# Kernel optimization log

Hardware: AMD Instinct MI355X
Metric: run time of the kernel (lower is better)

The kernel has to match this reference:

```python
import jax, jax.numpy as jnp
import numpy as np

B, S, H, V, C = 32, 512, 256, 50000, 5
NUM_LAYERS, WINDOW = 2, 2


def setup_inputs() -> dict:
    key = jax.random.key(0)
    ks = jax.random.split(key, 24)
    std = 0.1  # matches nn.init.normal_(p, 0, 0.1)
    n = lambda k, shp: jax.random.normal(k, shp, dtype=jnp.float32) * std
    u = lambda k, shp: -0.05 + jax.random.uniform(k, shp, dtype=jnp.float32) * 0.1
    return {
        "input_sentences": jax.random.randint(ks[0], (B, S), 0, V),
        "sentences_length": jax.random.randint(ks[1], (B,), 1, S),
        "hh0": u(ks[2], (B, S, H)),
        "cs0": u(ks[3], (B, S, H)),
        "embed": n(ks[4], (V, H)),
        # stacked word-gate weights, gate order: i, l, r, f, s, output, u
        "W_lr": n(ks[5], (7, H, 2 * H)),
        "W_c": n(ks[6], (7, H, H)),
        "W_x": n(ks[7], (7, H, H)),
        "W_g": n(ks[8], (7, H, H)),
        "gate_bias": n(ks[9], (7, H)),
        # sentence-state gates
        "W_fg_g": n(ks[10], (H, H)),
        "W_fg_h": n(ks[11], (H, H)),
        "W_fgi_g": n(ks[12], (H, H)),
        "W_fgi_h": n(ks[13], (H, H)),
        "W_og_g": n(ks[14], (H, H)),
        "W_og_h": n(ks[15], (H, H)),
        "b_fg": n(ks[16], (H,)),
        "b_fgi": n(ks[17], (H,)),
        # output head
        "W1": n(ks[18], (H, 2 * H)),
        "b1": n(ks[19], (H,)),
        "Wout": n(ks[20], (C, H)),
        "bout": n(ks[21], (C,)),
    }


def _before_sum(x, window):
    # sum of right-shifted (zero-padded at front) copies, shifts 1..window
    out = jnp.zeros_like(x)
    for s in range(1, window + 1):
        out = out + jnp.pad(x[:, :-s], ((0, 0), (s, 0), (0, 0)))
    return out


def _after_sum(x, window):
    out = jnp.zeros_like(x)
    for s in range(1, window + 1):
        out = out + jnp.pad(x[:, s:], ((0, 0), (0, s), (0, 0)))
    return out


def _slstm_step(hh, cs, sv, scs, wv, W_lr, W_c, W_x, W_g, gate_bias,
                W_fg_g, W_fg_h, W_fgi_g, W_fgi_h, W_og_g, W_og_h, b_fg, b_fgi):
    avg_hh = hh.mean(axis=1)                                   # [B,H]
    f_hat_g = jax.nn.sigmoid(sv @ W_fg_g.T + avg_hh @ W_fg_h.T + b_fg)
    # NOTE: original code (faithfully) uses output_gate_bias here, not output_gate_g_bias
    og_g = jax.nn.sigmoid(sv @ W_og_g.T + avg_hh @ W_og_h.T + gate_bias[5])
    f_hat_g_i = jax.nn.sigmoid((sv @ W_fgi_g.T)[:, None] + hh @ W_fgi_h.T + b_fgi)
    scores = jax.nn.softmax(f_hat_g_i, axis=2)                 # over hidden dim
    new_scs = jax.nn.softmax(f_hat_g, axis=1) * scs + (scores * cs).sum(axis=1)
    new_sv = og_g * jnp.tanh(new_scs)

    hb = _before_sum(hh, WINDOW)
    ha = _after_sum(hh, WINDOW)
    cb = _before_sum(cs, WINDOW)
    ca = _after_sum(cs, WINDOW)
    ba = jnp.concatenate([hb, ha], axis=-1)                    # [B,S,2H]

    # all 7 gate pre-activations at once: [B,S,7,H]
    pre = (jnp.einsum('bsk,ghk->bsgh', ba, W_lr)
           + jnp.einsum('bsk,ghk->bsgh', hh, W_c)
           + jnp.einsum('bsk,ghk->bsgh', wv, W_x)
           + (jnp.einsum('bk,ghk->bgh', new_sv, W_g) + gate_bias)[:, None])

    g5 = jax.nn.sigmoid(pre[..., :5, :])                       # i,l,r,f,s
    b_, s_ = g5.shape[:2]
    # joint softmax over the concatenated 5*H gate vector (as in torch cat+softmax)
    g5 = jax.nn.softmax(g5.reshape(b_, s_, -1), axis=-1).reshape(b_, s_, 5, -1)
    i_t, l_t, r_t, f_t, s_t = (g5[..., k, :] for k in range(5))
    og = jax.nn.sigmoid(pre[..., 5, :])
    u_g = jnp.tanh(pre[..., 6, :])

    new_cs = l_t * cb + f_t * cs + r_t * ca + s_t * scs[:, None] + i_t * u_g
    new_hh = og * jnp.tanh(new_cs)
    return new_hh, new_cs, new_sv, new_scs


def reference(input_sentences, sentences_length, hh0, cs0, embed,
              W_lr, W_c, W_x, W_g, gate_bias,
              W_fg_g, W_fg_h, W_fgi_g, W_fgi_h, W_og_g, W_og_h, b_fg, b_fgi,
              W1, b1, Wout, bout):
    wv = embed[input_sentences]                                # [B,S,H]
    hh, cs = hh0, cs0
    sv, scs = hh0.mean(axis=1), cs0.mean(axis=1)
    for _ in range(NUM_LAYERS):
        hh, cs, sv, scs = _slstm_step(hh, cs, sv, scs, wv,
                                      W_lr, W_c, W_x, W_g, gate_bias,
                                      W_fg_g, W_fg_h, W_fgi_g, W_fgi_h,
                                      W_og_g, W_og_h, b_fg, b_fgi)
    avg_hh = hh.mean(axis=1)
    conc = jnp.concatenate([avg_hh, sv], axis=1) @ W1.T + b1
    fc = conc @ Wout.T + bout
    return jax.nn.log_softmax(fc, axis=1), sv
```

## Files before the change

### kernel.cpp

```cpp
#include <hip/hip_runtime.h>
#include <stdint.h>
#include <math.h>

#define B_   32
#define S_   512
#define H_   256
#define M_   (B_*S_)
#define KBIG 1024
#define NB   1792
#define C_   5

typedef __bf16 bf16;
typedef __bf16 bf16x8 __attribute__((ext_vector_type(8)));
typedef float  floatx4 __attribute__((ext_vector_type(4)));

__device__ __forceinline__ float sigm(float x){ return 1.f/(1.f+expf(-x)); }

__device__ __forceinline__ void gl16(const bf16* g, bf16* l){
    __builtin_amdgcn_global_load_lds(
        (const __attribute__((address_space(1))) unsigned int*)g,
        (__attribute__((address_space(3))) unsigned int*)l, 16, 0, 0);
}

__global__ void wcomb_k(const float* __restrict__ Wlr, const float* __restrict__ Wc,
                        const float* __restrict__ Wx, bf16* __restrict__ WT){
    int n = blockIdx.x;
    int g = n >> 8, h = n & 255;
    int k4 = threadIdx.x * 4;
    const float* src;
    if (k4 < 512)      src = Wlr + ((size_t)(g*256 + h))*512 + k4;
    else if (k4 < 768) src = Wc  + ((size_t)(g*256 + h))*256 + (k4 - 512);
    else               src = Wx  + ((size_t)(g*256 + h))*256 + (k4 - 768);
    float4 v = *(const float4*)src;
    bf16 o[4] = {(bf16)v.x,(bf16)v.y,(bf16)v.z,(bf16)v.w};
    *(uint2*)&WT[(size_t)n*KBIG + k4] = *(uint2*)o;
}

__global__ void cvtw_k(const float* __restrict__ a, bf16* __restrict__ o){
    int i4 = (blockIdx.x*256 + threadIdx.x)*4;
    float4 v = *(const float4*)(a + i4);
    bf16 t[4] = {(bf16)v.x,(bf16)v.y,(bf16)v.z,(bf16)v.w};
    *(uint2*)(o + i4) = *(uint2*)t;
}

__global__ void gather_k(const int* __restrict__ idx, const float* __restrict__ embed,
                         bf16* __restrict__ wv){
    int i4 = (blockIdx.x*256 + threadIdx.x)*4;
    int m = i4 >> 8, h = i4 & 255;
    float4 v = *(const float4*)(embed + (size_t)idx[m]*H_ + h);
    bf16 o[4] = {(bf16)v.x,(bf16)v.y,(bf16)v.z,(bf16)v.w};
    *(uint2*)(wv + (size_t)m*H_ + h) = *(uint2*)o;
}

__global__ void mean1_k(const float* __restrict__ x, float* __restrict__ part){
    int b = blockIdx.x, c = blockIdx.y, h = threadIdx.x;
    const float* p = x + ((size_t)b*S_ + c*32)*H_ + h;
    float s = 0.f;
    #pragma unroll 8
    for (int t=0;t<32;t++) s += p[(size_t)t*H_];
    part[((size_t)b*16 + c)*H_ + h] = s;
}
__global__ void mean2_k(const float* __restrict__ part, float* __restrict__ out){
    int b = blockIdx.x, h = threadIdx.x;
    float s = 0.f;
    #pragma unroll
    for (int c=0;c<16;c++) s += part[((size_t)b*16 + c)*H_ + h];
    out[b*H_ + h] = s * (1.f/512.f);
}

__global__ void buildx_k(const float* __restrict__ hh, const bf16* __restrict__ wv,
                         bf16* __restrict__ X){
    int m = blockIdx.x, h = threadIdx.x;
    int s = m & (S_-1);
    size_t base = (size_t)m*H_ + h;
    float hb = (s>=1    ? hh[base - H_] : 0.f) + (s>=2    ? hh[base - 2*H_] : 0.f);
    float ha = (s<=S_-2 ? hh[base + H_] : 0.f) + (s<=S_-3 ? hh[base + 2*H_] : 0.f);
    bf16* xr = X + (size_t)m*KBIG;
    xr[h]     = (bf16)hb;
    xr[256+h] = (bf16)ha;
    xr[512+h] = (bf16)hh[base];
    xr[768+h] = wv[base];
}

__global__ void mv5_k(const float* __restrict__ sv, const float* __restrict__ avg,
    const float* __restrict__ Wfg_g, const float* __restrict__ Wfg_h,
    const float* __restrict__ Wog_g, const float* __restrict__ Wog_h,
    const float* __restrict__ Wfgi_g, float* __restrict__ res){
    int j = blockIdx.x, b = blockIdx.y, h = threadIdx.x;
    const float* vec = (j==1 || j==3) ? avg + b*H_ : sv + b*H_;
    const float* W   = (j==0)?Wfg_g:(j==1)?Wfg_h:(j==2)?Wog_g:(j==3)?Wog_h:Wfgi_g;
    __shared__ float v[H_];
    v[h] = vec[h]; __syncthreads();
    const float* w = W + (size_t)h*H_;
    float d = 0.f;
    for (int k=0;k<H_;k++) d += v[k]*w[k];
    res[((size_t)b*5 + j)*H_ + h] = d;
}
__global__ void comb_k(const float* __restrict__ res, const float* __restrict__ b_fg,
                       const float* __restrict__ gbias, const float* __restrict__ b_fgi,
                       float* __restrict__ fhg, float* __restrict__ ogg,
                       float* __restrict__ svg){
    int b = blockIdx.x, h = threadIdx.x;
    const float* r = res + (size_t)b*5*H_;
    fhg[b*H_+h] = sigm(r[h] + r[H_+h] + b_fg[h]);
    ogg[b*H_+h] = sigm(r[2*H_+h] + r[3*H_+h] + gbias[5*H_+h]);
    svg[b*H_+h] = r[4*H_+h] + b_fgi[h];
}

template<int EPI>
__global__ __launch_bounds__(256)
void mgemm_k(const bf16* __restrict__ A, const bf16* __restrict__ BT,
             bf16* __restrict__ C, const float* __restrict__ gt,
             int Kdim, int lda, int ldb, int ldc){
    __shared__ alignas(16) bf16 lsA[128*32];
    __shared__ alignas(16) bf16 lsB[128*32];
    int tid  = threadIdx.x;
    int m0 = blockIdx.y * 128, n0 = blockIdx.x * 128;
    int wave = tid >> 6, lane = tid & 63;
    int wm = (wave & 1) * 64, wn = (wave >> 1) * 64;
    int lrow = lane & 15, quad = lane >> 4;

    floatx4 zero = {0.f,0.f,0.f,0.f};
    floatx4 acc[4][4];
    #pragma unroll
    for (int i=0;i<4;i++)
        #pragma unroll
        for (int j=0;j<4;j++) acc[i][j] = zero;

    int srow = tid >> 2;
    int scol = (tid & 3) * 8;
    const bf16* Abase = A  + (size_t)(m0 + srow)*lda + scol;
    const bf16* Bbase = BT + (size_t)(n0 + srow)*ldb + scol;
    bf16* dA0 = &lsA[srow*32 + scol];
    bf16* dA1 = &lsA[(64+srow)*32 + scol];
    bf16* dB0 = &lsB[srow*32 + scol];
    bf16* dB1 = &lsB[(64+srow)*32 + scol];

    for (int k0 = 0; k0 < Kdim; k0 += 32){
        __syncthreads();
        gl16(Abase + k0,                     dA0);
        gl16(Abase + (size_t)64*lda + k0,    dA1);
        gl16(Bbase + k0,                     dB0);
        gl16(Bbase + (size_t)64*ldb + k0,    dB1);
        __syncthreads();
        bf16x8 af[4], bfr[4];
        #pragma unroll
        for (int mi=0;mi<4;mi++) af[mi]  = *(const bf16x8*)&lsA[(wm+mi*16+lrow)*32 + quad*8];
        #pragma unroll
        for (int ni=0;ni<4;ni++) bfr[ni] = *(const bf16x8*)&lsB[(wn+ni*16+lrow)*32 + quad*8];
        #pragma unroll
        for (int mi=0;mi<4;mi++)
            #pragma unroll
            for (int ni=0;ni<4;ni++)
                acc[mi][ni] = __builtin_amdgcn_mfma_f32_16x16x32_bf16(af[mi], bfr[ni], acc[mi][ni], 0, 0, 0);
    }

    #pragma unroll
    for (int mi=0;mi<4;mi++)
        #pragma unroll
        for (int ni=0;ni<4;ni++){
            int row = m0 + wm + mi*16 + quad*4;
            int col = n0 + wn + ni*16 + lrow;
            #pragma unroll
            for (int r=0;r<4;r++){
                float v = acc[mi][ni][r];
                if (EPI) v += gt[(size_t)((row+r)>>9)*NB + col];
                C[(size_t)(row+r)*ldc + col] = (bf16)v;
            }
        }
}

__global__ void scorep_k(const bf16* __restrict__ fgih, const float* __restrict__ svg,
                         const float* __restrict__ cs, float* __restrict__ part){
    int chunk = blockIdx.x, b = blockIdx.y;
    int tid = threadIdx.x, wave = tid >> 6, lane = tid & 63;
    __shared__ float acc4[4][256];
    float sw[4], acc[4] = {0.f,0.f,0.f,0.f};
    #pragma unroll
    for (int j=0;j<4;j++) sw[j] = svg[b*H_ + lane + 64*j];
    for (int t=wave; t<16; t+=4){
        int m = b*S_ + chunk*16 + t;
        const bf16* fr = fgih + (size_t)m*H_;
        float e[4], loc = 0.f;
        #pragma unroll
        for (int j=0;j<4;j++){ e[j] = expf(sigm(sw[j] + (float)fr[lane+64*j])); loc += e[j]; }
        #pragma unroll
        for (int off=32; off; off>>=1) loc += __shfl_xor(loc, off, 64);
        float inv = 1.f/loc;
        const float* cr = cs + (size_t)m*H_;
        #pragma unroll
        for (int j=0;j<4;j++) acc[j] += e[j]*inv*cr[lane+64*j];
    }
    #pragma unroll
    for (int j=0;j<4;j++) acc4[wave][lane+64*j] = acc[j];
    __syncthreads();
    part[((size_t)b*32 + chunk)*H_ + tid] =
        acc4[0][tid] + acc4[1][tid] + acc4[2][tid] + acc4[3][tid];
}

__global__ void newscs_k(const float* __restrict__ part, const float* __restrict__ fhg,
                         const float* __restrict__ ogg, const float* __restrict__ scs_in,
                         float* __restrict__ scs_out, float* __restrict__ sv_out){
    int b = blockIdx.x, h = threadIdx.x;
    __shared__ float r[256];
    float dot = 0.f;
    #pragma unroll 8
    for (int c=0;c<32;c++) dot += part[((size_t)b*32+c)*H_ + h];
    float e = expf(fhg[b*H_+h]);
    r[h] = e; __syncthreads();
    for (int off=128; off; off>>=1){ if (h<off) r[h] += r[h+off]; __syncthreads(); }
    float ns = (e / r[0]) * scs_in[b*H_+h] + dot;
    scs_out[b*H_+h] = ns;
    sv_out[b*H_+h]  = ogg[b*H_+h] * tanhf(ns);
}

__global__ void gterm_k(const float* __restrict__ svn, const float* __restrict__ Wg,
                        const float* __restrict__ gbias, float* __restrict__ gt){
    int g = blockIdx.x, b = blockIdx.y, h = threadIdx.x;
    __shared__ float s[H_];
    s[h] = svn[b*H_+h]; __syncthreads();
    const float* w = Wg + ((size_t)g*H_ + h)*H_;
    float d = 0.f;
    for (int k=0;k<H_;k++) d += s[k]*w[k];
    gt[(size_t)b*NB + g*H_ + h] = d + gbias[g*H_+h];
}

__global__ void gates_k(const bf16* __restrict__ pre, const float* __restrict__ cs_in,
                        const float* __restrict__ scs_in,
                        float* __restrict__ hh_out, float* __restrict__ cs_out){
    int tid = threadIdx.x, wave = tid >> 6, lane = tid & 63;
    int m = blockIdx.x*4 + wave;
    int b = m >> 9, s = m & (S_-1);
    const bf16* row = pre + (size_t)m*NB;
    float ex[4][5], og[4], u[4];
    float loc = 0.f;
    #pragma unroll
    for (int j=0;j<4;j++){
        int h = lane + 64*j;
        #pragma unroll
        for (int g=0; g<5; ++g){
            float e = expf(sigm((float)row[g*H_ + h]));
            ex[j][g] = e; loc += e;
        }
        og[j] = sigm((float)row[5*H_ + h]);
        u[j]  = tanhf((float)row[6*H_ + h]);
    }
    #pragma unroll
    for (int off=32; off; off>>=1) loc += __shfl_xor(loc, off, 64);
    float inv = 1.f / loc;
    #pragma unroll
    for (int j=0;j<4;j++){
        int h = lane + 64*j;
        size_t i = (size_t)m*H_ + h;
        float cb = (s>=1    ? cs_in[i - H_] : 0.f) + (s>=2    ? cs_in[i - 2*H_] : 0.f);
        float ca = (s<=S_-2 ? cs_in[i + H_] : 0.f) + (s<=S_-3 ? cs_in[i + 2*H_] : 0.f);
        float nc = ex[j][1]*inv*cb + ex[j][3]*inv*cs_in[i] + ex[j][2]*inv*ca
                 + ex[j][4]*inv*scs_in[b*H_+h] + ex[j][0]*inv*u[j];
        cs_out[i] = nc;
        hh_out[i] = og[j] * tanhf(nc);
    }
}

__global__ void head_k(const float* __restrict__ avgh, const float* __restrict__ sv,
                       const float* __restrict__ W1, const float* __restrict__ b1,
                       const float* __restrict__ Wout, const float* __restrict__ bout,
                       float* __restrict__ out){
    int b = blockIdx.x, t = threadIdx.x;
    __shared__ float conc[H_];
    __shared__ float fc[8];
    const float* wr = W1 + (size_t)t*512;
    float d = b1[t];
    for (int k=0;k<H_;k++) d += avgh[b*H_+k]*wr[k];
    for (int k=0;k<H_;k++) d += sv[b*H_+k]*wr[256+k];
    conc[t] = d;
    __syncthreads();
    if (t < C_){
        const float* wo = Wout + (size_t)t*H_;
        float s = bout[t];
        for (int i=0;i<H_;i++) s += conc[i]*wo[i];
        fc[t] = s;
    }
    __syncthreads();
    if (t == 0){
        float mx = fc[0];
        for (int c=1;c<C_;c++) mx = fmaxf(mx, fc[c]);
        float se = 0.f;
        for (int c=0;c<C_;c++) se += expf(fc[c]-mx);
        float lse = mx + logf(se);
        for (int c=0;c<C_;c++) out[b*C_+c] = fc[c]-lse;
    }
    out[B_*C_ + b*H_ + t] = sv[b*H_+t];
}

extern "C" void kernel_launch(void* const* d_in, const int* in_sizes, int n_in,
                              void* d_out, int out_size, void* d_ws, size_t ws_size,
                              hipStream_t stream){
    const int*   idx    = (const int*)d_in[0];
    const float* hh0    = (const float*)d_in[2];
    const float* cs0    = (const float*)d_in[3];
    const float* embed  = (const float*)d_in[4];
    const float* Wlr    = (const float*)d_in[5];
    const float* Wc     = (const float*)d_in[6];
    const float* Wx     = (const float*)d_in[7];
    const float* Wg     = (const float*)d_in[8];
    const float* gbias  = (const float*)d_in[9];
    const float* Wfg_g  = (const float*)d_in[10];
    const float* Wfg_h  = (const float*)d_in[11];
    const float* Wfgi_g = (const float*)d_in[12];
    const float* Wfgi_h = (const float*)d_in[13];
    const float* Wog_g  = (const float*)d_in[14];
    const float* Wog_h  = (const float*)d_in[15];
    const float* b_fg   = (const float*)d_in[16];
    const float* b_fgi  = (const float*)d_in[17];
    const float* W1     = (const float*)d_in[18];
    const float* b1     = (const float*)d_in[19];
    const float* Wout   = (const float*)d_in[20];
    const float* bout   = (const float*)d_in[21];

    uint8_t* p = (uint8_t*)d_ws;
    auto alloc = [&](size_t bytes)->void*{ void* r=(void*)p; p += (bytes + 255) & ~(size_t)255; return r; };
    bf16*  WT    = (bf16*)alloc((size_t)NB*KBIG*2);
    bf16*  WfgiT = (bf16*)alloc((size_t)H_*H_*2);
    bf16*  X     = (bf16*)alloc((size_t)M_*KBIG*2);
    bf16*  wv    = (bf16*)alloc((size_t)M_*H_*2);
    bf16*  pre   = (bf16*)alloc((size_t)M_*NB*2);
    bf16*  fgih  = (bf16*)alloc((size_t)M_*H_*2);
    float* hhA = (float*)alloc((size_t)M_*H_*4);
    float* csA = (float*)alloc((size_t)M_*H_*4);
    float* hhB = (float*)alloc((size_t)M_*H_*4);
    float* csB = (float*)alloc((size_t)M_*H_*4);
    float* mpart= (float*)alloc((size_t)B_*16*H_*4);
    float* part = (float*)alloc((size_t)B_*32*H_*4);
    float* res5 = (float*)alloc((size_t)B_*5*H_*4);
    float* avgh = (float*)alloc(B_*H_*4);
    float* fhg  = (float*)alloc(B_*H_*4);
    float* ogg  = (float*)alloc(B_*H_*4);
    float* svg  = (float*)alloc(B_*H_*4);
    float* svP0 = (float*)alloc(B_*H_*4);
    float* svP1 = (float*)alloc(B_*H_*4);
    float* scP0 = (float*)alloc(B_*H_*4);
    float* scP1 = (float*)alloc(B_*H_*4);
    float* gt   = (float*)alloc((size_t)B_*NB*4);

    wcomb_k <<<NB,          256, 0, stream>>>(Wlr, Wc, Wx, WT);
    cvtw_k  <<<(H_*H_)/1024,256, 0, stream>>>(Wfgi_h, WfgiT);
    gather_k<<<(M_*H_)/1024,256, 0, stream>>>(idx, embed, wv);
    mean1_k <<<dim3(B_,16), 256, 0, stream>>>(hh0, mpart);
    mean2_k <<<B_,          256, 0, stream>>>(mpart, svP0);
    mean1_k <<<dim3(B_,16), 256, 0, stream>>>(cs0, mpart);
    mean2_k <<<B_,          256, 0, stream>>>(mpart, scP0);

    const float *hin = hh0, *cin = cs0;
    float *hout = hhA, *cout = csA;
    float *svin = svP0, *scin = scP0, *svout = svP1, *scout = scP1;

    for (int l=0; l<2; ++l){
        const float* avgp;
        if (l == 0){
            avgp = svin;
        } else {
            mean1_k<<<dim3(B_,16), 256, 0, stream>>>(hin, mpart);
            mean2_k<<<B_,          256, 0, stream>>>(mpart, avgh);
            avgp = avgh;
        }
        mv5_k   <<<dim3(5,B_), 256, 0, stream>>>(svin, avgp, Wfg_g, Wfg_h, Wog_g,
                                                 Wog_h, Wfgi_g, res5);
        comb_k  <<<B_, 256, 0, stream>>>(res5, b_fg, gbias, b_fgi, fhg, ogg, svg);
        buildx_k<<<M_, 256, 0, stream>>>(hin, wv, X);
        mgemm_k<0><<<dim3(2,128), 256, 0, stream>>>(X+512, WfgiT, fgih, nullptr,
                                                    H_, KBIG, H_, H_);
        scorep_k<<<dim3(32,B_), 256, 0, stream>>>(fgih, svg, cin, part);
        newscs_k<<<B_, 256, 0, stream>>>(part, fhg, ogg, scin, scout, svout);
        gterm_k <<<dim3(7,B_), 256, 0, stream>>>(svout, Wg, gbias, gt);
        mgemm_k<1><<<dim3(14,128), 256, 0, stream>>>(X, WT, pre, gt,
                                                     KBIG, KBIG, KBIG, NB);
        gates_k <<<M_/4, 256, 0, stream>>>(pre, cin, scin, hout, cout);
        hin = hout; cin = cout;
        hout = (l==0) ? hhB : hhA;
        cout = (l==0) ? csB : csA;
        float* q;
        q = svin; svin = svout; svout = q;
        q = scin; scin = scout; scout = q;
    }
    mean1_k<<<dim3(B_,16), 256, 0, stream>>>(hin, mpart);
    mean2_k<<<B_,          256, 0, stream>>>(mpart, avgh);
    head_k <<<B_, 256, 0, stream>>>(avgh, svin, W1, b1, Wout, bout, (float*)d_out);
}
```

Before: 571.1 us.

## Replace main gate GEMM with 256x256-tile 8-wave double-buffered MFMA kernel

Adds a new GEMM kernel for the large gate projection (M=16384, N=1792, K=1024) that uses 256x256 output tiles, 512 threads and double-buffered LDS filled with direct global-to-LDS loads. Loads are interleaved in quarter steps with explicit vmcnt waits, barriers and setprio around the MFMA clusters, and LDS reads use an XOR swizzle. The epilogue bias term is hoisted because each tile lies within a single batch row. The larger tiles raise data reuse per block, at the cost of 128KB LDS per block and a grid of only 448 blocks, which may leave the 256 CUs unevenly loaded.

```diff
diff --git a/kernel.cpp b/kernel.cpp
--- a/kernel.cpp
+++ b/kernel.cpp
@@ -165,6 +165,132 @@
             for (int r=0;r<4;r++){
                 float v = acc[mi][ni][r];
                 if (EPI) v += gt[(size_t)((row+r)>>9)*NB + col];
+                C[(size_t)(row+r)*ldc + col] = (bf16)v;
+            }
+        }
+}
+
+template<int EPI>
+__device__ __forceinline__ void mmq(floatx4 (&acc)[8][4], bf16x8 (&af)[4][2], bf16x8 (&bfr)[2][2],
+                                    int MH, int NH){
+    #pragma unroll
+    for (int mi2=0;mi2<4;mi2++)
+        #pragma unroll
+        for (int ni2=0;ni2<2;ni2++)
+            #pragma unroll
+            for (int kk=0;kk<2;kk++)
+                acc[MH*4+mi2][NH*2+ni2] = __builtin_amdgcn_mfma_f32_16x16x32_bf16(
+                    af[mi2][kk], bfr[ni2][kk], acc[MH*4+mi2][NH*2+ni2], 0, 0, 0);
+}
+
+template<int EPI>
+__global__ __launch_bounds__(512, 2)
+void mgemm256_k(const bf16* __restrict__ A, const bf16* __restrict__ BT,
+                bf16* __restrict__ C, const float* __restrict__ gt,
+                int Kdim, int lda, int ldb, int ldc){
+    __shared__ alignas(16) bf16 lsA[2][256*64];
+    __shared__ alignas(16) bf16 lsB[2][256*64];
+    const int tid  = threadIdx.x;
+    const int lane = tid & 63;
+    const int wave = tid >> 6;
+    const int wm = wave >> 2;
+    const int wn = wave & 3;
+    const int lrow = lane & 15, quad = lane >> 4;
+    const int m0 = blockIdx.y * 256, n0 = blockIdx.x * 256;
+
+    const int srow = tid >> 3;
+    const int scol = ((tid & 7) ^ (srow & 7)) * 8;
+    const bf16* Ab = A  + (size_t)(m0 + srow)*lda + scol;
+    const bf16* Bb = BT + (size_t)(n0 + srow)*ldb + scol;
+    const int NT = Kdim >> 6;
+
+    floatx4 zero = {0.f,0.f,0.f,0.f};
+    floatx4 acc[8][4];
+    #pragma unroll
+    for (int i=0;i<8;i++)
+        #pragma unroll
+        for (int j=0;j<4;j++) acc[i][j] = zero;
+    bf16x8 af[4][2], bfr[2][2];
+
+#define SA_(bu,r,kt) gl16(Ab + (size_t)(r)*64*lda + (size_t)(kt)*64, &lsA[bu][(r)*4096 + tid*8])
+#define SB_(bu,r,kt) gl16(Bb + (size_t)(r)*64*ldb + (size_t)(kt)*64, &lsB[bu][(r)*4096 + tid*8])
+#define RA_(bu,MH,mi2,kk) (*(const bf16x8*)&lsA[bu][(wm*128 + (MH)*64 + (mi2)*16 + lrow)*64 + ((((kk)*4+quad) ^ (lrow&7))*8)])
+#define RB_(bu,NH,ni2,kk) (*(const bf16x8*)&lsB[bu][(wn*64  + (NH)*32 + (ni2)*16 + lrow)*64 + ((((kk)*4+quad) ^ (lrow&7))*8)])
+
+    SB_(0,0,0); SB_(0,1,0); SB_(0,2,0); SB_(0,3,0);
+    SA_(0,0,0); SA_(0,2,0); SA_(0,1,0); SA_(0,3,0);
+    asm volatile("s_waitcnt vmcnt(2)" ::: "memory");
+    __builtin_amdgcn_s_barrier();
+
+    #pragma unroll 2
+    for (int kt = 0; kt < NT; ++kt){
+        const int cur = kt & 1, nxt = cur ^ 1;
+        const bool st = (kt + 1 < NT);
+        const int k1 = kt + 1;
+
+        if (st){ SB_(nxt,0,k1); SB_(nxt,1,k1); }
+        #pragma unroll
+        for (int mi2=0;mi2<4;mi2++){ af[mi2][0] = RA_(cur,0,mi2,0); af[mi2][1] = RA_(cur,0,mi2,1); }
+        #pragma unroll
+        for (int ni2=0;ni2<2;ni2++){ bfr[ni2][0] = RB_(cur,0,ni2,0); bfr[ni2][1] = RB_(cur,0,ni2,1); }
+        __builtin_amdgcn_s_barrier();
+        __builtin_amdgcn_s_setprio(1);
+        mmq<EPI>(acc, af, bfr, 0, 0);
+        __builtin_amdgcn_s_setprio(0);
+        __builtin_amdgcn_s_barrier();
+
+        if (st){ SB_(nxt,2,k1); SB_(nxt,3,k1); }
+        #pragma unroll
+        for (int ni2=0;ni2<2;ni2++){ bfr[ni2][0] = RB_(cur,1,ni2,0); bfr[ni2][1] = RB_(cur,1,ni2,1); }
+        __builtin_amdgcn_s_barrier();
+        __builtin_amdgcn_s_setprio(1);
+        mmq<EPI>(acc, af, bfr, 0, 1);
+        __builtin_amdgcn_s_setprio(0);
+        if (st) asm volatile("s_waitcnt vmcnt(4)" ::: "memory");
+        else    asm volatile("s_waitcnt vmcnt(0)" ::: "memory");
+        __builtin_amdgcn_s_barrier();
+
+        if (st){ SA_(nxt,0,k1); SA_(nxt,2,k1); }
+        #pragma unroll
+        for (int mi2=0;mi2<4;mi2++){ af[mi2][0] = RA_(cur,1,mi2,0); af[mi2][1] = RA_(cur,1,mi2,1); }
+        __builtin_amdgcn_s_barrier();
+        __builtin_amdgcn_s_setprio(1);
+        mmq<EPI>(acc, af, bfr, 1, 1);
+        __builtin_amdgcn_s_setprio(0);
+        __builtin_amdgcn_s_barrier();
+
+        if (st){ SA_(nxt,1,k1); SA_(nxt,3,k1); }
+        #pragma unroll
+        for (int ni2=0;ni2<2;ni2++){ bfr[ni2][0] = RB_(cur,0,ni2,0); bfr[ni2][1] = RB_(cur,0,ni2,1); }
+        __builtin_amdgcn_s_barrier();
+        __builtin_amdgcn_s_setprio(1);
+        mmq<EPI>(acc, af, bfr, 1, 0);
+        __builtin_amdgcn_s_setprio(0);
+        asm volatile("s_waitcnt vmcnt(2)" ::: "memory");
+        __builtin_amdgcn_s_barrier();
+    }
+#undef SA_
+#undef SB_
+#undef RA_
+#undef RB_
+
+    float gtv[4] = {0.f,0.f,0.f,0.f};
+    if (EPI){
+        const int b = m0 >> 9;
+        #pragma unroll
+        for (int ni=0;ni<4;ni++)
+            gtv[ni] = gt[(size_t)b*NB + n0 + wn*64 + ni*16 + lrow];
+    }
+    #pragma unroll
+    for (int mi=0;mi<8;mi++)
+        #pragma unroll
+        for (int ni=0;ni<4;ni++){
+            int row = m0 + wm*128 + mi*16 + quad*4;
+            int col = n0 + wn*64  + ni*16 + lrow;
+            #pragma unroll
+            for (int r=0;r<4;r++){
+                float v = acc[mi][ni][r];
+                if (EPI) v += gtv[ni];
                 C[(size_t)(row+r)*ldc + col] = (bf16)v;
             }
         }
@@ -372,8 +498,8 @@
         scorep_k<<<dim3(32,B_), 256, 0, stream>>>(fgih, svg, cin, part);
         newscs_k<<<B_, 256, 0, stream>>>(part, fhg, ogg, scin, scout, svout);
         gterm_k <<<dim3(7,B_), 256, 0, stream>>>(svout, Wg, gbias, gt);
-        mgemm_k<1><<<dim3(14,128), 256, 0, stream>>>(X, WT, pre, gt,
-                                                     KBIG, KBIG, KBIG, NB);
+        mgemm256_k<1><<<dim3(7,64), 512, 0, stream>>>(X, WT, pre, gt,
+                                                      KBIG, KBIG, KBIG, NB);
         gates_k <<<M_/4, 256, 0, stream>>>(pre, cin, scin, hout, cout);
         hin = hout; cin = cout;
         hout = (l==0) ? hhB : hhA;
```

Result: slower. 594.2 us (+4.0%).
